# Kernel optimization log

Measured on AMD Instinct MI355X. Metric: run time of the kernel, lower is better.

The kernel has to match this reference:

```python
import jax, jax.numpy as jnp
import numpy as np

E = 1024

def setup_inputs() -> dict:
    key = jax.random.key(0)
    ks = jax.random.split(key, 7)
    s = 1.0 / np.sqrt(E)
    x = jax.random.normal(ks[0], (16, 2048, E), dtype=jnp.float32)
    Wq = jax.random.uniform(ks[1], (E, E), jnp.float32, -s, s)
    bq = jax.random.uniform(ks[2], (E,), jnp.float32, -s, s)
    Wk = jax.random.uniform(ks[3], (E, E), jnp.float32, -s, s)
    bk = jax.random.uniform(ks[4], (E,), jnp.float32, -s, s)
    Wv = jax.random.uniform(ks[5], (E, E), jnp.float32, -s, s)
    bv = jax.random.uniform(ks[6], (E,), jnp.float32, -s, s)
    return {"x": x, "Wq": Wq, "bq": bq, "Wk": Wk, "bk": bk, "Wv": Wv, "bv": bv}

def reference(x, Wq, bq, Wk, bk, Wv, bv):
    # torch Linear: y = x @ W.T + b, W is [out, in]
    q = jnp.einsum('bse,oe->bso', x, Wq) + bq
    k = jnp.einsum('bse,oe->bso', x, Wk) + bk
    v = jnp.einsum('bse,oe->bso', x, Wv) + bv
    scale = 1.0 / jnp.sqrt(jnp.asarray(Wq.shape[1], x.dtype))  # query.weight.shape[1]
    scores = jnp.einsum('bsd,btd->bst', q, k) * scale  # [B, S, S]
    weights = jax.nn.softmax(scores, axis=-1)          # dropout = identity (eval)
    out = jnp.einsum('bst,btd->bsd', weights, v)
    return out
```

## Files before the change

### kernel.cpp

```cpp
#include <hip/hip_runtime.h>
#include <hip/hip_bf16.h>

#define B_ 16
#define S_ 2048
#define E_ 1024
#define M_ (B_ * S_)

typedef unsigned short u16;
typedef float f32x4 __attribute__((ext_vector_type(4)));
typedef short s16x8 __attribute__((ext_vector_type(8)));
typedef unsigned short u16x8 __attribute__((ext_vector_type(8)));

__device__ __forceinline__ u16 f2bf(float f) {
    __hip_bfloat16 h = __float2bfloat16(f);
    return *reinterpret_cast<u16*>(&h);
}

__device__ __forceinline__ float bf2f(u16 v) {
    unsigned u = ((unsigned)v) << 16;
    return __uint_as_float(u);
}

__device__ __forceinline__ void gload_lds16(const void* g, void* lds) {
    __builtin_amdgcn_global_load_lds(
        (const __attribute__((address_space(1))) void*)g,
        (__attribute__((address_space(3))) void*)lds, 16, 0, 0);
}

__global__ __launch_bounds__(256) void cvt_f32_bf16(const float* __restrict__ src,
                                                    u16* __restrict__ dst, int n8) {
    for (int i = blockIdx.x * 256 + threadIdx.x; i < n8; i += gridDim.x * 256) {
        const float4* sp = (const float4*)src + (size_t)i * 2;
        float4 a = sp[0], b = sp[1];
        u16x8 o;
        o[0] = f2bf(a.x); o[1] = f2bf(a.y); o[2] = f2bf(a.z); o[3] = f2bf(a.w);
        o[4] = f2bf(b.x); o[5] = f2bf(b.y); o[6] = f2bf(b.z); o[7] = f2bf(b.w);
        *((u16x8*)dst + i) = o;
    }
}

template <int KLEN>
__device__ __forceinline__ void gemm_tile_core(const u16* __restrict__ Abase,
                                               const u16* __restrict__ Bbase,
                                               u16* sA, u16* sB, f32x4 acc[4][4], int t) {
    const int w = t >> 6, lane = t & 63;
    const int wr = w >> 1, wc = w & 1;
    const int lrow = lane & 15, lk = (lane >> 4) * 8;

    for (int k0 = 0; k0 < KLEN; k0 += 32) {
#pragma unroll
        for (int i = 0; i < 2; ++i) {
            int o = w * 1024 + i * 4096 + lane * 16;
            int row = o >> 6, colb = o & 63;
            gload_lds16((const char*)Abase + (size_t)row * (KLEN * 2) + (size_t)k0 * 2 + colb,
                        (char*)sA + w * 1024 + i * 4096);
            gload_lds16((const char*)Bbase + (size_t)row * (KLEN * 2) + (size_t)k0 * 2 + colb,
                        (char*)sB + w * 1024 + i * 4096);
        }
        __syncthreads();
        s16x8 av[4], bv[4];
#pragma unroll
        for (int mi = 0; mi < 4; ++mi)
            av[mi] = *(const s16x8*)&sA[(wr * 64 + mi * 16 + lrow) * 32 + lk];
#pragma unroll
        for (int ni = 0; ni < 4; ++ni)
            bv[ni] = *(const s16x8*)&sB[(wc * 64 + ni * 16 + lrow) * 32 + lk];
#pragma unroll
        for (int mi = 0; mi < 4; ++mi)
#pragma unroll
            for (int ni = 0; ni < 4; ++ni)
                acc[mi][ni] =
                    __builtin_amdgcn_mfma_f32_16x16x32_bf16(av[mi], bv[ni], acc[mi][ni], 0, 0, 0);
        __syncthreads();
    }
}

__device__ __forceinline__ int xcd_swizzle(int bid, int nwg) {
    int cpx = nwg >> 3;
    return (bid & 7) * cpx + (bid >> 3);
}

__global__ __launch_bounds__(256) void gemm_qkv(const u16* __restrict__ xb,
                                                const u16* __restrict__ Wb,
                                                const float* __restrict__ bq,
                                                const float* __restrict__ bk,
                                                const float* __restrict__ bvp,
                                                u16* __restrict__ qkv) {
    __shared__ u16 sA[4096], sB[4096];
    int wg = xcd_swizzle(blockIdx.x, 256 * 24);
    int mt = wg / 24, nt = wg % 24;
    const u16* Ab = xb + (size_t)mt * 128 * E_;
    const u16* Bb = Wb + (size_t)nt * 128 * E_;
    f32x4 zero = {0.f, 0.f, 0.f, 0.f};
    f32x4 acc[4][4];
#pragma unroll
    for (int i = 0; i < 4; ++i)
#pragma unroll
        for (int j = 0; j < 4; ++j) acc[i][j] = zero;
    gemm_tile_core<E_>(Ab, Bb, sA, sB, acc, threadIdx.x);

    int t = threadIdx.x, w = t >> 6, lane = t & 63, wr = w >> 1, wc = w & 1;
    int mat = nt / 8;
    const float* bias = (mat == 0) ? bq : ((mat == 1) ? bk : bvp);
#pragma unroll
    for (int ni = 0; ni < 4; ++ni) {
        int n = nt * 128 + wc * 64 + ni * 16 + (lane & 15);
        int col = n & 1023;
        float bb = bias[col];
#pragma unroll
        for (int mi = 0; mi < 4; ++mi)
#pragma unroll
            for (int j = 0; j < 4; ++j) {
                int m = mt * 128 + wr * 64 + mi * 16 + (lane >> 4) * 4 + j;
                qkv[((size_t)mat * M_ + m) * E_ + col] = f2bf(acc[mi][ni][j] + bb);
            }
    }
}

__global__ __launch_bounds__(256) void transpose_v(const u16* __restrict__ V,
                                                   u16* __restrict__ vt) {
    int bid = blockIdx.x;
    int b = bid >> 9;
    int rem = bid & 511;
    int jt = rem >> 4, dt = rem & 15;
    __shared__ u16 lds[64 * 65];
    int t = threadIdx.x;
#pragma unroll
    for (int p = 0; p < 2; ++p) {
        int e = p * 2048 + t * 8;
        int j = e >> 6, d0 = e & 63;
        u16x8 v = *(const u16x8*)&V[((size_t)b * S_ + jt * 64 + j) * E_ + dt * 64 + d0];
#pragma unroll
        for (int q = 0; q < 8; ++q) lds[j * 65 + d0 + q] = v[q];
    }
    __syncthreads();
#pragma unroll
    for (int p = 0; p < 2; ++p) {
        int e = p * 2048 + t * 8;
        int d = e >> 6, j0 = e & 63;
        u16x8 o;
#pragma unroll
        for (int q = 0; q < 8; ++q) o[q] = lds[(j0 + q) * 65 + d];
        *(u16x8*)&vt[((size_t)b * E_ + dt * 64 + d) * S_ + jt * 64 + j0] = o;
    }
}

__global__ __launch_bounds__(256) void gemm_sexp(const u16* __restrict__ qkv,
                                                 u16* __restrict__ Pbuf,
                                                 float* __restrict__ lsum, int b0) {
    __shared__ u16 sA[4096], sB[4096];
    int wg = xcd_swizzle(blockIdx.x, gridDim.x);
    int ci = wg >> 8;
    int rem = wg & 255;
    int mt = rem >> 4, nt = rem & 15;
    int b = b0 + ci;
    const u16* Q = qkv + ((size_t)b * S_ + mt * 128) * E_;
    const u16* K = qkv + (size_t)M_ * E_ + ((size_t)b * S_ + nt * 128) * E_;
    f32x4 zero = {0.f, 0.f, 0.f, 0.f};
    f32x4 acc[4][4];
#pragma unroll
    for (int i = 0; i < 4; ++i)
#pragma unroll
        for (int j = 0; j < 4; ++j) acc[i][j] = zero;
    gemm_tile_core<E_>(Q, K, sA, sB, acc, threadIdx.x);

    int t = threadIdx.x, w = t >> 6, lane = t & 63, wr = w >> 1, wc = w & 1;
#pragma unroll
    for (int mi = 0; mi < 4; ++mi) {
#pragma unroll
        for (int j = 0; j < 4; ++j) {
            int m = mt * 128 + wr * 64 + mi * 16 + (lane >> 4) * 4 + j;
            size_t base = ((size_t)ci * S_ + m) * S_;
            float psum = 0.f;
            u16 pb[4];
#pragma unroll
            for (int ni = 0; ni < 4; ++ni) {
                float p = __expf(acc[mi][ni][j] * 0.03125f);
                u16 pv = f2bf(p);
                pb[ni] = pv;
                psum += bf2f(pv);
            }
#pragma unroll
            for (int ni = 0; ni < 4; ++ni) {
                int n = nt * 128 + wc * 64 + ni * 16 + (lane & 15);
                Pbuf[base + n] = pb[ni];
            }
            psum += __shfl_xor(psum, 1, 64);
            psum += __shfl_xor(psum, 2, 64);
            psum += __shfl_xor(psum, 4, 64);
            psum += __shfl_xor(psum, 8, 64);
            if ((lane & 15) == 0) atomicAdd(&lsum[(size_t)b * S_ + m], psum);
        }
    }
}

__global__ __launch_bounds__(256) void gemm_pv(const u16* __restrict__ Pbuf,
                                               const u16* __restrict__ vt,
                                               const float* __restrict__ lsum,
                                               float* __restrict__ out, int b0) {
    __shared__ u16 sA[4096], sB[4096];
    int wg = xcd_swizzle(blockIdx.x, gridDim.x);
    int ci = wg >> 7;
    int rem = wg & 127;
    int mt = rem >> 3, nt = rem & 7;
    int b = b0 + ci;
    const u16* A = Pbuf + (size_t)ci * S_ * S_ + (size_t)mt * 128 * S_;
    const u16* Bb = vt + ((size_t)b * E_ + nt * 128) * S_;
    f32x4 zero = {0.f, 0.f, 0.f, 0.f};
    f32x4 acc[4][4];
#pragma unroll
    for (int i = 0; i < 4; ++i)
#pragma unroll
        for (int j = 0; j < 4; ++j) acc[i][j] = zero;
    gemm_tile_core<S_>(A, Bb, sA, sB, acc, threadIdx.x);

    int t = threadIdx.x, w = t >> 6, lane = t & 63, wr = w >> 1, wc = w & 1;
#pragma unroll
    for (int mi = 0; mi < 4; ++mi) {
#pragma unroll
        for (int j = 0; j < 4; ++j) {
            int m = mt * 128 + wr * 64 + mi * 16 + (lane >> 4) * 4 + j;
            float inv = 1.0f / lsum[(size_t)b * S_ + m];
#pragma unroll
            for (int ni = 0; ni < 4; ++ni) {
                int n = nt * 128 + wc * 64 + ni * 16 + (lane & 15);
                out[((size_t)b * S_ + m) * E_ + n] = acc[mi][ni][j] * inv;
            }
        }
    }
}

extern "C" void kernel_launch(void* const* d_in, const int* in_sizes, int n_in,
                              void* d_out, int out_size, void* d_ws, size_t ws_size,
                              hipStream_t stream) {
    const float* x = (const float*)d_in[0];
    const float* Wq = (const float*)d_in[1];
    const float* bq = (const float*)d_in[2];
    const float* Wk = (const float*)d_in[3];
    const float* bk = (const float*)d_in[4];
    const float* Wv = (const float*)d_in[5];
    const float* bv = (const float*)d_in[6];
    float* out = (float*)d_out;

    char* ws = (char*)d_ws;
    const size_t xb_off = 0;
    const size_t wb_off = xb_off + (size_t)M_ * E_ * 2;
    const size_t qkv_off = wb_off + (size_t)3 * E_ * E_ * 2;
    const size_t vt_off = qkv_off + (size_t)3 * M_ * E_ * 2;
    const size_t l_off = vt_off + (size_t)M_ * E_ * 2;
    const size_t chunk_off = l_off + (size_t)M_ * 4;

    u16* xb = (u16*)(ws + xb_off);
    u16* Wb = (u16*)(ws + wb_off);
    u16* qkv = (u16*)(ws + qkv_off);
    u16* vt = (u16*)(ws + vt_off);
    float* lsum = (float*)(ws + l_off);

    int CH = 16;
    while (CH > 1 && chunk_off + (size_t)CH * S_ * S_ * 2 > ws_size) CH >>= 1;
    u16* Pbuf = (u16*)(ws + chunk_off);

    hipMemsetAsync(lsum, 0, (size_t)M_ * 4, stream);

    cvt_f32_bf16<<<2048, 256, 0, stream>>>(x, xb, M_ * E_ / 8);
    cvt_f32_bf16<<<512, 256, 0, stream>>>(Wq, Wb, E_ * E_ / 8);
    cvt_f32_bf16<<<512, 256, 0, stream>>>(Wk, Wb + E_ * E_, E_ * E_ / 8);
    cvt_f32_bf16<<<512, 256, 0, stream>>>(Wv, Wb + 2 * E_ * E_, E_ * E_ / 8);

    gemm_qkv<<<256 * 24, 256, 0, stream>>>(xb, Wb, bq, bk, bv, qkv);
    transpose_v<<<16 * 32 * 16, 256, 0, stream>>>(qkv + (size_t)2 * M_ * E_, vt);

    for (int b0 = 0; b0 < B_; b0 += CH) {
        gemm_sexp<<<CH * 256, 256, 0, stream>>>(qkv, Pbuf, lsum, b0);
        gemm_pv<<<CH * 128, 256, 0, stream>>>(Pbuf, vt, lsum, out, b0);
    }
}
```

Baseline: 936.4 us.

## Replace 128x128 GEMM core with pipelined 256x256 tile, swizzled LDS, 8 waves

Swaps the shared GEMM core for a 256x256 output tile per 512-thread block with K-step 64. Global-to-LDS loads are double-buffered and interleaved with four MFMA quadrants, using explicit waitcnt, barriers and setprio. LDS columns are XOR-swizzled to avoid bank conflicts. Larger tiles raise arithmetic intensity and cut global traffic, and the pipelining hides load latency. The cost is 128KB of LDS, more accumulator registers and fewer blocks in flight.

```diff
diff --git a/kernel.cpp b/kernel.cpp
--- a/kernel.cpp
+++ b/kernel.cpp
@@ -39,84 +39,6 @@
     }
 }
 
-template <int KLEN>
-__device__ __forceinline__ void gemm_tile_core(const u16* __restrict__ Abase,
-                                               const u16* __restrict__ Bbase,
-                                               u16* sA, u16* sB, f32x4 acc[4][4], int t) {
-    const int w = t >> 6, lane = t & 63;
-    const int wr = w >> 1, wc = w & 1;
-    const int lrow = lane & 15, lk = (lane >> 4) * 8;
-
-    for (int k0 = 0; k0 < KLEN; k0 += 32) {
-#pragma unroll
-        for (int i = 0; i < 2; ++i) {
-            int o = w * 1024 + i * 4096 + lane * 16;
-            int row = o >> 6, colb = o & 63;
-            gload_lds16((const char*)Abase + (size_t)row * (KLEN * 2) + (size_t)k0 * 2 + colb,
-                        (char*)sA + w * 1024 + i * 4096);
-            gload_lds16((const char*)Bbase + (size_t)row * (KLEN * 2) + (size_t)k0 * 2 + colb,
-                        (char*)sB + w * 1024 + i * 4096);
-        }
-        __syncthreads();
-        s16x8 av[4], bv[4];
-#pragma unroll
-        for (int mi = 0; mi < 4; ++mi)
-            av[mi] = *(const s16x8*)&sA[(wr * 64 + mi * 16 + lrow) * 32 + lk];
-#pragma unroll
-        for (int ni = 0; ni < 4; ++ni)
-            bv[ni] = *(const s16x8*)&sB[(wc * 64 + ni * 16 + lrow) * 32 + lk];
-#pragma unroll
-        for (int mi = 0; mi < 4; ++mi)
-#pragma unroll
-            for (int ni = 0; ni < 4; ++ni)
-                acc[mi][ni] =
-                    __builtin_amdgcn_mfma_f32_16x16x32_bf16(av[mi], bv[ni], acc[mi][ni], 0, 0, 0);
-        __syncthreads();
-    }
-}
-
-__device__ __forceinline__ int xcd_swizzle(int bid, int nwg) {
-    int cpx = nwg >> 3;
-    return (bid & 7) * cpx + (bid >> 3);
-}
-
-__global__ __launch_bounds__(256) void gemm_qkv(const u16* __restrict__ xb,
-                                                const u16* __restrict__ Wb,
-                                                const float* __restrict__ bq,
-                                                const float* __restrict__ bk,
-                                                const float* __restrict__ bvp,
-                                                u16* __restrict__ qkv) {
-    __shared__ u16 sA[4096], sB[4096];
-    int wg = xcd_swizzle(blockIdx.x, 256 * 24);
-    int mt = wg / 24, nt = wg % 24;
-    const u16* Ab = xb + (size_t)mt * 128 * E_;
-    const u16* Bb = Wb + (size_t)nt * 128 * E_;
-    f32x4 zero = {0.f, 0.f, 0.f, 0.f};
-    f32x4 acc[4][4];
-#pragma unroll
-    for (int i = 0; i < 4; ++i)
-#pragma unroll
-        for (int j = 0; j < 4; ++j) acc[i][j] = zero;
-    gemm_tile_core<E_>(Ab, Bb, sA, sB, acc, threadIdx.x);
-
-    int t = threadIdx.x, w = t >> 6, lane = t & 63, wr = w >> 1, wc = w & 1;
-    int mat = nt / 8;
-    const float* bias = (mat == 0) ? bq : ((mat == 1) ? bk : bvp);
-#pragma unroll
-    for (int ni = 0; ni < 4; ++ni) {
-        int n = nt * 128 + wc * 64 + ni * 16 + (lane & 15);
-        int col = n & 1023;
-        float bb = bias[col];
-#pragma unroll
-        for (int mi = 0; mi < 4; ++mi)
-#pragma unroll
-            for (int j = 0; j < 4; ++j) {
-                int m = mt * 128 + wr * 64 + mi * 16 + (lane >> 4) * 4 + j;
-                qkv[((size_t)mat * M_ + m) * E_ + col] = f2bf(acc[mi][ni][j] + bb);
-            }
-    }
-}
-
 __global__ __launch_bounds__(256) void transpose_v(const u16* __restrict__ V,
                                                    u16* __restrict__ vt) {
     int bid = blockIdx.x;
@@ -145,89 +67,260 @@
     }
 }
 
-__global__ __launch_bounds__(256) void gemm_sexp(const u16* __restrict__ qkv,
-                                                 u16* __restrict__ Pbuf,
-                                                 float* __restrict__ lsum, int b0) {
-    __shared__ u16 sA[4096], sB[4096];
+__device__ __forceinline__ int xcd_swizzle(int bid, int nwg) {
+    int cpx = nwg >> 3;
+    return (bid & 7) * cpx + (bid >> 3);
+}
+
+template <int KLEN>
+__device__ __forceinline__ void gemm256_core(const u16* __restrict__ Abase,
+                                             const u16* __restrict__ Bbase,
+                                             char* lds, f32x4 acc[8][4], int tid) {
+    constexpr int KT = KLEN / 64;
+    const int w = tid >> 6, lane = tid & 63;
+    const int wr = w >> 2, wc = w & 3;
+    const int lrow = lane & 15;
+    const int srow = lane >> 3;
+    const int scolb = ((lane & 7) ^ srow) << 4;
+    const int rsel = (lane >> 4) << 4;
+    const int rxor = (lane & 7) << 4;
+
+    auto stage = [&](int kt, int which) {
+        if (kt >= KT) return;
+        const char* mb = (const char*)((which >= 2) ? Abase : Bbase);
+        const int h = which & 1;
+        char* dst = lds + ((kt & 1) ? 65536 : 0) + ((which >= 2) ? 0 : 32768) +
+                    h * 16384 + w * 1024;
+#pragma unroll
+        for (int l = 0; l < 2; ++l) {
+            const int row = h * 128 + l * 64 + w * 8 + srow;
+            gload_lds16(mb + (size_t)row * (KLEN * 2) + kt * 128 + scolb, dst + l * 8192);
+        }
+    };
+
+    stage(0, 0); stage(0, 1); stage(0, 2); stage(0, 3);
+    stage(1, 0); stage(1, 1);
+    asm volatile("s_waitcnt vmcnt(4)" ::: "memory");
+    __builtin_amdgcn_s_barrier();
+
+    s16x8 a[4][2], b0[2][2], b1[2][2];
+#pragma unroll 1
+    for (int kt = 0; kt < KT; ++kt) {
+        const char* sA = lds + ((kt & 1) ? 65536 : 0);
+        const char* sB = sA + 32768;
+#pragma unroll
+        for (int mi = 0; mi < 4; ++mi) {
+            const int r = wr * 128 + mi * 16 + lrow;
+#pragma unroll
+            for (int ks = 0; ks < 2; ++ks)
+                a[mi][ks] = *(const s16x8*)(sA + r * 128 + ((ks * 64 + rsel) ^ rxor));
+        }
+#pragma unroll
+        for (int ni = 0; ni < 2; ++ni) {
+            const int c = wc * 64 + ni * 16 + lrow;
+#pragma unroll
+            for (int ks = 0; ks < 2; ++ks)
+                b0[ni][ks] = *(const s16x8*)(sB + c * 128 + ((ks * 64 + rsel) ^ rxor));
+        }
+        stage(kt + 1, 2);
+        __builtin_amdgcn_s_barrier();
+        asm volatile("s_waitcnt lgkmcnt(0)" ::: "memory");
+        __builtin_amdgcn_sched_barrier(0);
+        __builtin_amdgcn_s_setprio(1);
+#pragma unroll
+        for (int mi = 0; mi < 4; ++mi)
+#pragma unroll
+            for (int ni = 0; ni < 2; ++ni)
+#pragma unroll
+                for (int ks = 0; ks < 2; ++ks)
+                    acc[mi][ni] = __builtin_amdgcn_mfma_f32_16x16x32_bf16(
+                        a[mi][ks], b0[ni][ks], acc[mi][ni], 0, 0, 0);
+        __builtin_amdgcn_s_setprio(0);
+        __builtin_amdgcn_sched_barrier(0);
+        __builtin_amdgcn_s_barrier();
+#pragma unroll
+        for (int ni = 0; ni < 2; ++ni) {
+            const int c = wc * 64 + 32 + ni * 16 + lrow;
+#pragma unroll
+            for (int ks = 0; ks < 2; ++ks)
+                b1[ni][ks] = *(const s16x8*)(sB + c * 128 + ((ks * 64 + rsel) ^ rxor));
+        }
+        stage(kt + 1, 3);
+        __builtin_amdgcn_s_barrier();
+        asm volatile("s_waitcnt lgkmcnt(0)" ::: "memory");
+        __builtin_amdgcn_sched_barrier(0);
+        __builtin_amdgcn_s_setprio(1);
+#pragma unroll
+        for (int mi = 0; mi < 4; ++mi)
+#pragma unroll
+            for (int ni = 0; ni < 2; ++ni)
+#pragma unroll
+                for (int ks = 0; ks < 2; ++ks)
+                    acc[mi][2 + ni] = __builtin_amdgcn_mfma_f32_16x16x32_bf16(
+                        a[mi][ks], b1[ni][ks], acc[mi][2 + ni], 0, 0, 0);
+        __builtin_amdgcn_s_setprio(0);
+        __builtin_amdgcn_sched_barrier(0);
+        __builtin_amdgcn_s_barrier();
+#pragma unroll
+        for (int mi = 0; mi < 4; ++mi) {
+            const int r = wr * 128 + 64 + mi * 16 + lrow;
+#pragma unroll
+            for (int ks = 0; ks < 2; ++ks)
+                a[mi][ks] = *(const s16x8*)(sA + r * 128 + ((ks * 64 + rsel) ^ rxor));
+        }
+        stage(kt + 2, 0);
+        __builtin_amdgcn_s_barrier();
+        asm volatile("s_waitcnt lgkmcnt(0)" ::: "memory");
+        __builtin_amdgcn_sched_barrier(0);
+        __builtin_amdgcn_s_setprio(1);
+#pragma unroll
+        for (int mi = 0; mi < 4; ++mi)
+#pragma unroll
+            for (int ni = 0; ni < 2; ++ni)
+#pragma unroll
+                for (int ks = 0; ks < 2; ++ks)
+                    acc[4 + mi][ni] = __builtin_amdgcn_mfma_f32_16x16x32_bf16(
+                        a[mi][ks], b0[ni][ks], acc[4 + mi][ni], 0, 0, 0);
+        __builtin_amdgcn_s_setprio(0);
+        __builtin_amdgcn_sched_barrier(0);
+        __builtin_amdgcn_s_barrier();
+        stage(kt + 2, 1);
+        __builtin_amdgcn_s_barrier();
+        __builtin_amdgcn_sched_barrier(0);
+        __builtin_amdgcn_s_setprio(1);
+#pragma unroll
+        for (int mi = 0; mi < 4; ++mi)
+#pragma unroll
+            for (int ni = 0; ni < 2; ++ni)
+#pragma unroll
+                for (int ks = 0; ks < 2; ++ks)
+                    acc[4 + mi][2 + ni] = __builtin_amdgcn_mfma_f32_16x16x32_bf16(
+                        a[mi][ks], b1[ni][ks], acc[4 + mi][2 + ni], 0, 0, 0);
+        __builtin_amdgcn_s_setprio(0);
+        __builtin_amdgcn_sched_barrier(0);
+        if (kt == KT - 2) asm volatile("s_waitcnt vmcnt(0)" ::: "memory");
+        else               asm volatile("s_waitcnt vmcnt(4)" ::: "memory");
+        __builtin_amdgcn_s_barrier();
+    }
+}
+
+__global__ __launch_bounds__(512, 2) void gemm_qkv(const u16* __restrict__ xb,
+                                                   const u16* __restrict__ Wb,
+                                                   const float* __restrict__ bq,
+                                                   const float* __restrict__ bk,
+                                                   const float* __restrict__ bvp,
+                                                   u16* __restrict__ qkv) {
+    __shared__ f32x4 smem[8192];
+    char* lds = (char*)smem;
+    int wg = xcd_swizzle(blockIdx.x, 1536);
+    int mt = wg / 12, nt = wg % 12;
+    f32x4 acc[8][4];
+    f32x4 zero = {0.f, 0.f, 0.f, 0.f};
+#pragma unroll
+    for (int i = 0; i < 8; ++i)
+#pragma unroll
+        for (int j = 0; j < 4; ++j) acc[i][j] = zero;
+    gemm256_core<E_>(xb + (size_t)mt * 256 * E_, Wb + (size_t)nt * 256 * E_, lds, acc,
+                     threadIdx.x);
+
+    int tid = threadIdx.x, w = tid >> 6, lane = tid & 63, wr = w >> 2, wc = w & 3;
+    int mat = nt >> 2;
+    const float* bias = (mat == 0) ? bq : ((mat == 1) ? bk : bvp);
+    u16* outm = qkv + (size_t)mat * M_ * E_;
+    int bn = (nt & 3) * 256;
+#pragma unroll
+    for (int b = 0; b < 4; ++b) {
+        int n = bn + wc * 64 + (b >> 1) * 32 + (b & 1) * 16 + (lane & 15);
+        float bb = bias[n];
+#pragma unroll
+        for (int a = 0; a < 8; ++a)
+#pragma unroll
+            for (int j = 0; j < 4; ++j) {
+                int m = mt * 256 + wr * 128 + (a >> 2) * 64 + (a & 3) * 16 +
+                        ((lane >> 4) << 2) + j;
+                outm[(size_t)m * E_ + n] = f2bf(acc[a][b][j] + bb);
+            }
+    }
+}
+
+__global__ __launch_bounds__(512, 2) void gemm_sexp(const u16* __restrict__ qkv,
+                                                    u16* __restrict__ Pbuf,
+                                                    float* __restrict__ lsum, int b0) {
+    __shared__ f32x4 smem[8192];
+    char* lds = (char*)smem;
     int wg = xcd_swizzle(blockIdx.x, gridDim.x);
-    int ci = wg >> 8;
-    int rem = wg & 255;
-    int mt = rem >> 4, nt = rem & 15;
-    int b = b0 + ci;
-    const u16* Q = qkv + ((size_t)b * S_ + mt * 128) * E_;
-    const u16* K = qkv + (size_t)M_ * E_ + ((size_t)b * S_ + nt * 128) * E_;
+    int ci = wg >> 6, rem = wg & 63, mt = rem >> 3, ntt = rem & 7;
+    int bb = b0 + ci;
+    const u16* Q = qkv + ((size_t)bb * S_ + mt * 256) * E_;
+    const u16* K = qkv + (size_t)M_ * E_ + ((size_t)bb * S_ + ntt * 256) * E_;
+    f32x4 acc[8][4];
     f32x4 zero = {0.f, 0.f, 0.f, 0.f};
-    f32x4 acc[4][4];
-#pragma unroll
-    for (int i = 0; i < 4; ++i)
+#pragma unroll
+    for (int i = 0; i < 8; ++i)
 #pragma unroll
         for (int j = 0; j < 4; ++j) acc[i][j] = zero;
-    gemm_tile_core<E_>(Q, K, sA, sB, acc, threadIdx.x);
-
-    int t = threadIdx.x, w = t >> 6, lane = t & 63, wr = w >> 1, wc = w & 1;
-#pragma unroll
-    for (int mi = 0; mi < 4; ++mi) {
+    gemm256_core<E_>(Q, K, lds, acc, threadIdx.x);
+
+    int tid = threadIdx.x, w = tid >> 6, lane = tid & 63, wr = w >> 2, wc = w & 3;
+#pragma unroll
+    for (int a = 0; a < 8; ++a)
 #pragma unroll
         for (int j = 0; j < 4; ++j) {
-            int m = mt * 128 + wr * 64 + mi * 16 + (lane >> 4) * 4 + j;
+            int m = mt * 256 + wr * 128 + (a >> 2) * 64 + (a & 3) * 16 + ((lane >> 4) << 2) + j;
             size_t base = ((size_t)ci * S_ + m) * S_;
             float psum = 0.f;
             u16 pb[4];
 #pragma unroll
-            for (int ni = 0; ni < 4; ++ni) {
-                float p = __expf(acc[mi][ni][j] * 0.03125f);
-                u16 pv = f2bf(p);
-                pb[ni] = pv;
-                psum += bf2f(pv);
+            for (int b = 0; b < 4; ++b) {
+                float p = __expf(acc[a][b][j] * 0.03125f);
+                pb[b] = f2bf(p);
+                psum += bf2f(pb[b]);
             }
 #pragma unroll
-            for (int ni = 0; ni < 4; ++ni) {
-                int n = nt * 128 + wc * 64 + ni * 16 + (lane & 15);
-                Pbuf[base + n] = pb[ni];
+            for (int b = 0; b < 4; ++b) {
+                int n = ntt * 256 + wc * 64 + (b >> 1) * 32 + (b & 1) * 16 + (lane & 15);
+                Pbuf[base + n] = pb[b];
             }
             psum += __shfl_xor(psum, 1, 64);
             psum += __shfl_xor(psum, 2, 64);
             psum += __shfl_xor(psum, 4, 64);
             psum += __shfl_xor(psum, 8, 64);
-            if ((lane & 15) == 0) atomicAdd(&lsum[(size_t)b * S_ + m], psum);
-        }
-    }
-}
-
-__global__ __launch_bounds__(256) void gemm_pv(const u16* __restrict__ Pbuf,
-                                               const u16* __restrict__ vt,
-                                               const float* __restrict__ lsum,
-                                               float* __restrict__ out, int b0) {
-    __shared__ u16 sA[4096], sB[4096];
+            if ((lane & 15) == 0) atomicAdd(&lsum[(size_t)bb * S_ + m], psum);
+        }
+}
+
+__global__ __launch_bounds__(512, 2) void gemm_pv(const u16* __restrict__ Pbuf,
+                                                  const u16* __restrict__ vt,
+                                                  const float* __restrict__ lsum,
+                                                  float* __restrict__ out, int b0) {
+    __shared__ f32x4 smem[8192];
+    char* lds = (char*)smem;
     int wg = xcd_swizzle(blockIdx.x, gridDim.x);
-    int ci = wg >> 7;
-    int rem = wg & 127;
-    int mt = rem >> 3, nt = rem & 7;
-    int b = b0 + ci;
-    const u16* A = Pbuf + (size_t)ci * S_ * S_ + (size_t)mt * 128 * S_;
-    const u16* Bb = vt + ((size_t)b * E_ + nt * 128) * S_;
+    int ci = wg >> 5, rem = wg & 31, mt = rem >> 2, ntt = rem & 3;
+    int bb = b0 + ci;
+    const u16* A = Pbuf + (size_t)ci * S_ * S_ + (size_t)mt * 256 * S_;
+    const u16* Bb = vt + ((size_t)bb * E_ + ntt * 256) * S_;
+    f32x4 acc[8][4];
     f32x4 zero = {0.f, 0.f, 0.f, 0.f};
-    f32x4 acc[4][4];
-#pragma unroll
-    for (int i = 0; i < 4; ++i)
+#pragma unroll
+    for (int i = 0; i < 8; ++i)
 #pragma unroll
         for (int j = 0; j < 4; ++j) acc[i][j] = zero;
-    gemm_tile_core<S_>(A, Bb, sA, sB, acc, threadIdx.x);
-
-    int t = threadIdx.x, w = t >> 6, lane = t & 63, wr = w >> 1, wc = w & 1;
-#pragma unroll
-    for (int mi = 0; mi < 4; ++mi) {
+    gemm256_core<S_>(A, Bb, lds, acc, threadIdx.x);
+
+    int tid = threadIdx.x, w = tid >> 6, lane = tid & 63, wr = w >> 2, wc = w & 3;
+#pragma unroll
+    for (int a = 0; a < 8; ++a)
 #pragma unroll
         for (int j = 0; j < 4; ++j) {
-            int m = mt * 128 + wr * 64 + mi * 16 + (lane >> 4) * 4 + j;
-            float inv = 1.0f / lsum[(size_t)b * S_ + m];
-#pragma unroll
-            for (int ni = 0; ni < 4; ++ni) {
-                int n = nt * 128 + wc * 64 + ni * 16 + (lane & 15);
-                out[((size_t)b * S_ + m) * E_ + n] = acc[mi][ni][j] * inv;
+            int m = mt * 256 + wr * 128 + (a >> 2) * 64 + (a & 3) * 16 + ((lane >> 4) << 2) + j;
+            float inv = 1.0f / lsum[(size_t)bb * S_ + m];
+#pragma unroll
+            for (int b = 0; b < 4; ++b) {
+                int n = ntt * 256 + wc * 64 + (b >> 1) * 32 + (b & 1) * 16 + (lane & 15);
+                out[((size_t)bb * S_ + m) * E_ + n] = acc[a][b][j] * inv;
             }
         }
-    }
 }
 
 extern "C" void kernel_launch(void* const* d_in, const int* in_sizes, int n_in,
@@ -267,11 +360,11 @@
     cvt_f32_bf16<<<512, 256, 0, stream>>>(Wk, Wb + E_ * E_, E_ * E_ / 8);
     cvt_f32_bf16<<<512, 256, 0, stream>>>(Wv, Wb + 2 * E_ * E_, E_ * E_ / 8);
 
-    gemm_qkv<<<256 * 24, 256, 0, stream>>>(xb, Wb, bq, bk, bv, qkv);
+    gemm_qkv<<<1536, 512, 0, stream>>>(xb, Wb, bq, bk, bv, qkv);
     transpose_v<<<16 * 32 * 16, 256, 0, stream>>>(qkv + (size_t)2 * M_ * E_, vt);
 
     for (int b0 = 0; b0 < B_; b0 += CH) {
-        gemm_sexp<<<CH * 256, 256, 0, stream>>>(qkv, Pbuf, lsum, b0);
-        gemm_pv<<<CH * 128, 256, 0, stream>>>(Pbuf, vt, lsum, out, b0);
-    }
-}
+        gemm_sexp<<<CH * 64, 512, 0, stream>>>(qkv, Pbuf, lsum, b0);
+        gemm_pv<<<CH * 32, 512, 0, stream>>>(Pbuf, vt, lsum, out, b0);
+    }
+}
```

Measured after the change: 784.7 us. -16.2%, faster.

## Rework GEMM core with double-buffered LDS, XOR swizzle, and 256x128 tiles

Applied to the files above, without the earlier changes.

Replaces the shared GEMM tile loop with a version that double-buffers LDS, so the next k-slice is prefetched while MFMAs run on the current one. LDS rows get an XOR swizzle to avoid bank conflicts. Blocks grow to 512 threads covering 256x128 output tiles, which halves the grid sizes and raises A-tile reuse. It also raises MFMA priority with setprio and replaces __syncthreads with raw waitcnt plus barrier. The costs are more LDS per block (48KB), register pressure under launch_bounds(512,4), and hand-written synchronisation that must stay correct.

```diff
diff --git a/kernel.cpp b/kernel.cpp
--- a/kernel.cpp
+++ b/kernel.cpp
@@ -39,84 +39,6 @@
     }
 }
 
-template <int KLEN>
-__device__ __forceinline__ void gemm_tile_core(const u16* __restrict__ Abase,
-                                               const u16* __restrict__ Bbase,
-                                               u16* sA, u16* sB, f32x4 acc[4][4], int t) {
-    const int w = t >> 6, lane = t & 63;
-    const int wr = w >> 1, wc = w & 1;
-    const int lrow = lane & 15, lk = (lane >> 4) * 8;
-
-    for (int k0 = 0; k0 < KLEN; k0 += 32) {
-#pragma unroll
-        for (int i = 0; i < 2; ++i) {
-            int o = w * 1024 + i * 4096 + lane * 16;
-            int row = o >> 6, colb = o & 63;
-            gload_lds16((const char*)Abase + (size_t)row * (KLEN * 2) + (size_t)k0 * 2 + colb,
-                        (char*)sA + w * 1024 + i * 4096);
-            gload_lds16((const char*)Bbase + (size_t)row * (KLEN * 2) + (size_t)k0 * 2 + colb,
-                        (char*)sB + w * 1024 + i * 4096);
-        }
-        __syncthreads();
-        s16x8 av[4], bv[4];
-#pragma unroll
-        for (int mi = 0; mi < 4; ++mi)
-            av[mi] = *(const s16x8*)&sA[(wr * 64 + mi * 16 + lrow) * 32 + lk];
-#pragma unroll
-        for (int ni = 0; ni < 4; ++ni)
-            bv[ni] = *(const s16x8*)&sB[(wc * 64 + ni * 16 + lrow) * 32 + lk];
-#pragma unroll
-        for (int mi = 0; mi < 4; ++mi)
-#pragma unroll
-            for (int ni = 0; ni < 4; ++ni)
-                acc[mi][ni] =
-                    __builtin_amdgcn_mfma_f32_16x16x32_bf16(av[mi], bv[ni], acc[mi][ni], 0, 0, 0);
-        __syncthreads();
-    }
-}
-
-__device__ __forceinline__ int xcd_swizzle(int bid, int nwg) {
-    int cpx = nwg >> 3;
-    return (bid & 7) * cpx + (bid >> 3);
-}
-
-__global__ __launch_bounds__(256) void gemm_qkv(const u16* __restrict__ xb,
-                                                const u16* __restrict__ Wb,
-                                                const float* __restrict__ bq,
-                                                const float* __restrict__ bk,
-                                                const float* __restrict__ bvp,
-                                                u16* __restrict__ qkv) {
-    __shared__ u16 sA[4096], sB[4096];
-    int wg = xcd_swizzle(blockIdx.x, 256 * 24);
-    int mt = wg / 24, nt = wg % 24;
-    const u16* Ab = xb + (size_t)mt * 128 * E_;
-    const u16* Bb = Wb + (size_t)nt * 128 * E_;
-    f32x4 zero = {0.f, 0.f, 0.f, 0.f};
-    f32x4 acc[4][4];
-#pragma unroll
-    for (int i = 0; i < 4; ++i)
-#pragma unroll
-        for (int j = 0; j < 4; ++j) acc[i][j] = zero;
-    gemm_tile_core<E_>(Ab, Bb, sA, sB, acc, threadIdx.x);
-
-    int t = threadIdx.x, w = t >> 6, lane = t & 63, wr = w >> 1, wc = w & 1;
-    int mat = nt / 8;
-    const float* bias = (mat == 0) ? bq : ((mat == 1) ? bk : bvp);
-#pragma unroll
-    for (int ni = 0; ni < 4; ++ni) {
-        int n = nt * 128 + wc * 64 + ni * 16 + (lane & 15);
-        int col = n & 1023;
-        float bb = bias[col];
-#pragma unroll
-        for (int mi = 0; mi < 4; ++mi)
-#pragma unroll
-            for (int j = 0; j < 4; ++j) {
-                int m = mt * 128 + wr * 64 + mi * 16 + (lane >> 4) * 4 + j;
-                qkv[((size_t)mat * M_ + m) * E_ + col] = f2bf(acc[mi][ni][j] + bb);
-            }
-    }
-}
-
 __global__ __launch_bounds__(256) void transpose_v(const u16* __restrict__ V,
                                                    u16* __restrict__ vt) {
     int bid = blockIdx.x;
@@ -145,89 +67,191 @@
     }
 }
 
-__global__ __launch_bounds__(256) void gemm_sexp(const u16* __restrict__ qkv,
-                                                 u16* __restrict__ Pbuf,
-                                                 float* __restrict__ lsum, int b0) {
-    __shared__ u16 sA[4096], sB[4096];
+__device__ __forceinline__ int xcd_swizzle(int bid, int nwg) {
+    int cpx = nwg >> 3;
+    return (bid & 7) * cpx + (bid >> 3);
+}
+
+template <int KLEN>
+__device__ __forceinline__ void gemm_core(const u16* __restrict__ Abase,
+                                          const u16* __restrict__ Bbase,
+                                          char* lds, f32x4 acc[4][4], int tid) {
+    constexpr int KT = KLEN / 32;
+    const int w = tid >> 6, lane = tid & 63;
+    const int wr = w >> 1, wc = w & 1;
+    const int lr = lane & 15;
+    const int ch = lane >> 4;
+
+    auto stage = [&](int kt) {
+        if (kt >= KT) return;
+        char* base = lds + (kt & 1) * 24576;
+#pragma unroll
+        for (int i = 0; i < 2; ++i) {
+            int o = i * 8192 + tid * 16;
+            int row = o >> 6;
+            int sc = ((o >> 4) & 3) ^ ((row >> 1) & 3);
+            gload_lds16((const char*)Abase + (size_t)row * (KLEN * 2) + kt * 64 + sc * 16,
+                        base + i * 8192 + w * 1024);
+        }
+        {
+            int o = tid * 16;
+            int row = o >> 6;
+            int sc = ((o >> 4) & 3) ^ ((row >> 1) & 3);
+            gload_lds16((const char*)Bbase + (size_t)row * (KLEN * 2) + kt * 64 + sc * 16,
+                        base + 16384 + w * 1024);
+        }
+    };
+
+    stage(0);
+    asm volatile("s_waitcnt vmcnt(0)" ::: "memory");
+    __builtin_amdgcn_s_barrier();
+
+    s16x8 a[4], b[4];
+#pragma unroll 1
+    for (int kt = 0; kt < KT; ++kt) {
+        const char* sA = lds + (kt & 1) * 24576;
+        const char* sB = sA + 16384;
+#pragma unroll
+        for (int mi = 0; mi < 4; ++mi) {
+            const int r = wr * 64 + mi * 16 + lr;
+            a[mi] = *(const s16x8*)(sA + r * 64 + ((ch ^ ((r >> 1) & 3)) << 4));
+        }
+#pragma unroll
+        for (int ni = 0; ni < 4; ++ni) {
+            const int c = wc * 64 + ni * 16 + lr;
+            b[ni] = *(const s16x8*)(sB + c * 64 + ((ch ^ ((c >> 1) & 3)) << 4));
+        }
+        stage(kt + 1);
+        __builtin_amdgcn_s_setprio(1);
+#pragma unroll
+        for (int mi = 0; mi < 4; ++mi)
+#pragma unroll
+            for (int ni = 0; ni < 4; ++ni)
+                acc[mi][ni] = __builtin_amdgcn_mfma_f32_16x16x32_bf16(
+                    a[mi], b[ni], acc[mi][ni], 0, 0, 0);
+        __builtin_amdgcn_s_setprio(0);
+        asm volatile("s_waitcnt lgkmcnt(0)" ::: "memory");
+        asm volatile("s_waitcnt vmcnt(0)" ::: "memory");
+        __builtin_amdgcn_s_barrier();
+    }
+}
+
+__global__ __launch_bounds__(512, 4) void gemm_qkv(const u16* __restrict__ xb,
+                                                   const u16* __restrict__ Wb,
+                                                   const float* __restrict__ bq,
+                                                   const float* __restrict__ bk,
+                                                   const float* __restrict__ bvp,
+                                                   u16* __restrict__ qkv) {
+    __shared__ f32x4 smem[3072];
+    char* lds = (char*)smem;
+    int wg = xcd_swizzle(blockIdx.x, 3072);
+    int mt = wg / 24, nt = wg % 24;
+    f32x4 acc[4][4];
+    f32x4 zero = {0.f, 0.f, 0.f, 0.f};
+#pragma unroll
+    for (int i = 0; i < 4; ++i)
+#pragma unroll
+        for (int j = 0; j < 4; ++j) acc[i][j] = zero;
+    gemm_core<E_>(xb + (size_t)mt * 256 * E_, Wb + (size_t)nt * 128 * E_, lds, acc,
+                  threadIdx.x);
+
+    int tid = threadIdx.x, w = tid >> 6, lane = tid & 63, wr = w >> 1, wc = w & 1;
+    int mat = nt >> 3;
+    const float* bias = (mat == 0) ? bq : ((mat == 1) ? bk : bvp);
+    u16* outm = qkv + (size_t)mat * M_ * E_;
+    int bn = (nt & 7) * 128;
+#pragma unroll
+    for (int ni = 0; ni < 4; ++ni) {
+        int n = bn + wc * 64 + ni * 16 + (lane & 15);
+        float bb = bias[n];
+#pragma unroll
+        for (int mi = 0; mi < 4; ++mi)
+#pragma unroll
+            for (int j = 0; j < 4; ++j) {
+                int m = mt * 256 + wr * 64 + mi * 16 + ((lane >> 4) << 2) + j;
+                outm[(size_t)m * E_ + n] = f2bf(acc[mi][ni][j] + bb);
+            }
+    }
+}
+
+__global__ __launch_bounds__(512, 4) void gemm_sexp(const u16* __restrict__ qkv,
+                                                    u16* __restrict__ Pbuf,
+                                                    float* __restrict__ lsum, int b0) {
+    __shared__ f32x4 smem[3072];
+    char* lds = (char*)smem;
     int wg = xcd_swizzle(blockIdx.x, gridDim.x);
-    int ci = wg >> 8;
-    int rem = wg & 255;
-    int mt = rem >> 4, nt = rem & 15;
-    int b = b0 + ci;
-    const u16* Q = qkv + ((size_t)b * S_ + mt * 128) * E_;
-    const u16* K = qkv + (size_t)M_ * E_ + ((size_t)b * S_ + nt * 128) * E_;
+    int ci = wg >> 7, rem = wg & 127, mt = rem >> 4, ntt = rem & 15;
+    int bb = b0 + ci;
+    const u16* Q = qkv + ((size_t)bb * S_ + mt * 256) * E_;
+    const u16* K = qkv + (size_t)M_ * E_ + ((size_t)bb * S_ + ntt * 128) * E_;
+    f32x4 acc[4][4];
     f32x4 zero = {0.f, 0.f, 0.f, 0.f};
-    f32x4 acc[4][4];
 #pragma unroll
     for (int i = 0; i < 4; ++i)
 #pragma unroll
         for (int j = 0; j < 4; ++j) acc[i][j] = zero;
-    gemm_tile_core<E_>(Q, K, sA, sB, acc, threadIdx.x);
-
-    int t = threadIdx.x, w = t >> 6, lane = t & 63, wr = w >> 1, wc = w & 1;
-#pragma unroll
-    for (int mi = 0; mi < 4; ++mi) {
+    gemm_core<E_>(Q, K, lds, acc, threadIdx.x);
+
+    int tid = threadIdx.x, w = tid >> 6, lane = tid & 63, wr = w >> 1, wc = w & 1;
+#pragma unroll
+    for (int mi = 0; mi < 4; ++mi)
 #pragma unroll
         for (int j = 0; j < 4; ++j) {
-            int m = mt * 128 + wr * 64 + mi * 16 + (lane >> 4) * 4 + j;
+            int m = mt * 256 + wr * 64 + mi * 16 + ((lane >> 4) << 2) + j;
             size_t base = ((size_t)ci * S_ + m) * S_;
             float psum = 0.f;
             u16 pb[4];
 #pragma unroll
             for (int ni = 0; ni < 4; ++ni) {
                 float p = __expf(acc[mi][ni][j] * 0.03125f);
-                u16 pv = f2bf(p);
-                pb[ni] = pv;
-                psum += bf2f(pv);
+                pb[ni] = f2bf(p);
+                psum += bf2f(pb[ni]);
             }
 #pragma unroll
             for (int ni = 0; ni < 4; ++ni) {
-                int n = nt * 128 + wc * 64 + ni * 16 + (lane & 15);
+                int n = ntt * 128 + wc * 64 + ni * 16 + (lane & 15);
                 Pbuf[base + n] = pb[ni];
             }
             psum += __shfl_xor(psum, 1, 64);
             psum += __shfl_xor(psum, 2, 64);
             psum += __shfl_xor(psum, 4, 64);
             psum += __shfl_xor(psum, 8, 64);
-            if ((lane & 15) == 0) atomicAdd(&lsum[(size_t)b * S_ + m], psum);
-        }
-    }
-}
-
-__global__ __launch_bounds__(256) void gemm_pv(const u16* __restrict__ Pbuf,
-                                               const u16* __restrict__ vt,
-                                               const float* __restrict__ lsum,
-                                               float* __restrict__ out, int b0) {
-    __shared__ u16 sA[4096], sB[4096];
+            if ((lane & 15) == 0) atomicAdd(&lsum[(size_t)bb * S_ + m], psum);
+        }
+}
+
+__global__ __launch_bounds__(512, 4) void gemm_pv(const u16* __restrict__ Pbuf,
+                                                  const u16* __restrict__ vt,
+                                                  const float* __restrict__ lsum,
+                                                  float* __restrict__ out, int b0) {
+    __shared__ f32x4 smem[3072];
+    char* lds = (char*)smem;
     int wg = xcd_swizzle(blockIdx.x, gridDim.x);
-    int ci = wg >> 7;
-    int rem = wg & 127;
-    int mt = rem >> 3, nt = rem & 7;
-    int b = b0 + ci;
-    const u16* A = Pbuf + (size_t)ci * S_ * S_ + (size_t)mt * 128 * S_;
-    const u16* Bb = vt + ((size_t)b * E_ + nt * 128) * S_;
+    int ci = wg >> 6, rem = wg & 63, mt = rem >> 3, ntt = rem & 7;
+    int bb = b0 + ci;
+    const u16* A = Pbuf + (size_t)ci * S_ * S_ + (size_t)mt * 256 * S_;
+    const u16* Bb = vt + ((size_t)bb * E_ + ntt * 128) * S_;
+    f32x4 acc[4][4];
     f32x4 zero = {0.f, 0.f, 0.f, 0.f};
-    f32x4 acc[4][4];
 #pragma unroll
     for (int i = 0; i < 4; ++i)
 #pragma unroll
         for (int j = 0; j < 4; ++j) acc[i][j] = zero;
-    gemm_tile_core<S_>(A, Bb, sA, sB, acc, threadIdx.x);
-
-    int t = threadIdx.x, w = t >> 6, lane = t & 63, wr = w >> 1, wc = w & 1;
-#pragma unroll
-    for (int mi = 0; mi < 4; ++mi) {
+    gemm_core<S_>(A, Bb, lds, acc, threadIdx.x);
+
+    int tid = threadIdx.x, w = tid >> 6, lane = tid & 63, wr = w >> 1, wc = w & 1;
+#pragma unroll
+    for (int mi = 0; mi < 4; ++mi)
 #pragma unroll
         for (int j = 0; j < 4; ++j) {
-            int m = mt * 128 + wr * 64 + mi * 16 + (lane >> 4) * 4 + j;
-            float inv = 1.0f / lsum[(size_t)b * S_ + m];
+            int m = mt * 256 + wr * 64 + mi * 16 + ((lane >> 4) << 2) + j;
+            float inv = 1.0f / lsum[(size_t)bb * S_ + m];
 #pragma unroll
             for (int ni = 0; ni < 4; ++ni) {
-                int n = nt * 128 + wc * 64 + ni * 16 + (lane & 15);
-                out[((size_t)b * S_ + m) * E_ + n] = acc[mi][ni][j] * inv;
+                int n = ntt * 128 + wc * 64 + ni * 16 + (lane & 15);
+                out[((size_t)bb * S_ + m) * E_ + n] = acc[mi][ni][j] * inv;
             }
         }
-    }
 }
 
 extern "C" void kernel_launch(void* const* d_in, const int* in_sizes, int n_in,
@@ -267,11 +291,11 @@
     cvt_f32_bf16<<<512, 256, 0, stream>>>(Wk, Wb + E_ * E_, E_ * E_ / 8);
     cvt_f32_bf16<<<512, 256, 0, stream>>>(Wv, Wb + 2 * E_ * E_, E_ * E_ / 8);
 
-    gemm_qkv<<<256 * 24, 256, 0, stream>>>(xb, Wb, bq, bk, bv, qkv);
+    gemm_qkv<<<3072, 512, 0, stream>>>(xb, Wb, bq, bk, bv, qkv);
     transpose_v<<<16 * 32 * 16, 256, 0, stream>>>(qkv + (size_t)2 * M_ * E_, vt);
 
     for (int b0 = 0; b0 < B_; b0 += CH) {
-        gemm_sexp<<<CH * 256, 256, 0, stream>>>(qkv, Pbuf, lsum, b0);
-        gemm_pv<<<CH * 128, 256, 0, stream>>>(Pbuf, vt, lsum, out, b0);
-    }
-}
+        gemm_sexp<<<CH * 128, 512, 0, stream>>>(qkv, Pbuf, lsum, b0);
+        gemm_pv<<<CH * 64, 512, 0, stream>>>(Pbuf, vt, lsum, out, b0);
+    }
+}
```

Result: faster. 846.3 us (-9.6%).
